# Kernel tuning notes

Measured on AMD Instinct MI355X. Metric: run time of the kernel, lower is better.

## Reference

```python
import jax, jax.numpy as jnp
import numpy as np

B, SQ, SKV = 4, 2048, 2048
IN_Q, IN_KV = 1024, 1024
H, D = 16, 64            # num_heads, hidden_channels (per-head dim)
OUT = 1024
ROPE_BASE = 4096.0


def _rope(x, base):
    # x: (..., items, D). Interleaved rotate-half RoPE over last dim.
    d = x.shape[-1]
    s = x.shape[-2]
    inv_freq = base ** (-jnp.arange(0, d, 2, dtype=x.dtype) / d)      # (D/2,)
    ang = jnp.arange(s, dtype=x.dtype)[:, None] * inv_freq[None, :]   # (S, D/2)
    cos = jnp.repeat(jnp.cos(ang), 2, axis=-1)                        # (S, D)
    sin = jnp.repeat(jnp.sin(ang), 2, axis=-1)
    xp = x.reshape(x.shape[:-1] + (d // 2, 2))
    x_rot = jnp.stack([-xp[..., 1], xp[..., 0]], axis=-1).reshape(x.shape)
    return x * cos + x_rot * sin


def setup_inputs() -> dict:
    key = jax.random.key(0)
    ks = jax.random.split(key, 8)
    sc = 0.02
    return {
        "q": jax.random.normal(ks[0], (B, SQ, IN_Q), jnp.float32),
        "kv": jax.random.normal(ks[1], (B, SKV, IN_KV), jnp.float32),
        # weights stored (in, out): y = x @ W + b  (equiv. to torch Linear)
        "Wq": jax.random.normal(ks[2], (IN_Q, H * D), jnp.float32) * sc,
        "bq": jnp.zeros((H * D,), jnp.float32),
        "Wkv": jax.random.normal(ks[3], (IN_KV, 2 * D), jnp.float32) * sc,
        "bkv": jnp.zeros((2 * D,), jnp.float32),
        "Wo": jax.random.normal(ks[4], (H * D, OUT), jnp.float32) * sc,
        "bo": jnp.zeros((OUT,), jnp.float32),
    }


def reference(q, kv, Wq, bq, Wkv, bkv, Wo, bo):
    # Q projection -> (B, H, SQ, D)
    qh = (q @ Wq + bq).reshape(B, SQ, H, D).transpose(0, 2, 1, 3)
    # KV projection (multi-query: single shared K/V head) -> (B, SKV, D) each
    kvp = kv @ Wkv + bkv
    k, v = kvp[..., :D], kvp[..., D:]
    # Rotary positional encoding on the item axis
    qh = _rope(qh, ROPE_BASE)
    k = _rope(k, ROPE_BASE)
    # Scaled dot-product attention with broadcast single-head K/V (MQA)
    scale = 1.0 / jnp.sqrt(jnp.asarray(D, qh.dtype))
    scores = jnp.einsum("bhqd,bkd->bhqk", qh, k) * scale   # (B,H,SQ,SKV)
    attn = jax.nn.softmax(scores, axis=-1)
    h = jnp.einsum("bhqk,bkd->bhqd", attn, v)              # (B,H,SQ,D)
    # Merge heads and output projection
    h = h.transpose(0, 2, 1, 3).reshape(B, SQ, H * D)
    return h @ Wo + bo
```

## Files before the change

### kernel.cpp

```cpp
#include <hip/hip_runtime.h>
#include <math.h>

typedef __bf16 bf16;
typedef __bf16 bf16x4 __attribute__((ext_vector_type(4)));
typedef __bf16 bf16x8 __attribute__((ext_vector_type(8)));
typedef float floatx4 __attribute__((ext_vector_type(4)));

#define MFMA16(a, b, c) __builtin_amdgcn_mfma_f32_16x16x32_bf16(a, b, c, 0, 0, 0)

#if __has_builtin(__builtin_amdgcn_exp2f)
#define EXP2F(x) __builtin_amdgcn_exp2f(x)
#else
#define EXP2F(x) exp2f(x)
#endif

constexpr int Bc = 4, SQc = 2048, SKVc = 2048, Hc = 16, Dc = 64;
#define QSCALE 0.18033688011112042f

__device__ __forceinline__ void glds16(const bf16* g, bf16* lds_base, int lane) {
#if __has_builtin(__builtin_amdgcn_global_load_lds)
  __builtin_amdgcn_global_load_lds(
      (const __attribute__((address_space(1))) void*)g,
      (__attribute__((address_space(3))) void*)lds_base, 16, 0, 0);
#else
  *(bf16x8*)(lds_base + 8 * lane) = *(const bf16x8*)g;
#endif
}

__global__ void cvt_bf16(const float* __restrict__ in, bf16* __restrict__ out) {
  const size_t i = ((size_t)blockIdx.x * 256 + threadIdx.x) * 4;
  const float4 v = *(const float4*)&in[i];
  bf16x4 o = {(bf16)v.x, (bf16)v.y, (bf16)v.z, (bf16)v.w};
  *(bf16x4*)&out[i] = o;
}

__global__ void rope_tab_build(float2* __restrict__ tab) {
  const int i = blockIdx.x * 256 + threadIdx.x;
  const int pos = i >> 5, f = i & 31;
  const float ang = (float)pos * exp2f(-0.375f * (float)f);
  float sn, cs;
  sincosf(ang, &sn, &cs);
  tab[i] = make_float2(cs, sn);
}

__global__ void transpose_cvt(const float* __restrict__ in, bf16* __restrict__ out,
                              int K, int N) {
  __shared__ bf16 T[64][72];
  const int tid = threadIdx.x;
  const int n0 = blockIdx.x * 64, k0 = blockIdx.y * 64;
  const int tr = tid >> 4, tc4 = (tid & 15) * 4;
#pragma unroll
  for (int i = 0; i < 4; i++) {
    const int k = tr + 16 * i;
    const float4 v = *(const float4*)&in[(size_t)(k0 + k) * N + n0 + tc4];
    T[tc4 + 0][k] = (bf16)v.x;
    T[tc4 + 1][k] = (bf16)v.y;
    T[tc4 + 2][k] = (bf16)v.z;
    T[tc4 + 3][k] = (bf16)v.w;
  }
  __syncthreads();
  const int nr = tid >> 2, kc = (tid & 3) * 8;
#pragma unroll
  for (int hf = 0; hf < 2; hf++)
    *(bf16x8*)&out[(size_t)(n0 + nr) * K + k0 + kc + 32 * hf] =
        *(const bf16x8*)&T[nr][kc + 32 * hf];
}

__device__ __forceinline__ void gemm_kloop(const bf16* __restrict__ A,
                                           const bf16* __restrict__ BT, int m0,
                                           int n0, int tid, int wave, int lane,
                                           int m, int g, bf16 (*As)[128 * 64],
                                           bf16 (*Bs)[128 * 64],
                                           floatx4 (*acc)[4], int mq, int nq) {
  const int r_ = tid >> 3, p_ = tid & 7;
  const bf16* pA[4];
  const bf16* pB[4];
#pragma unroll
  for (int q = 0; q < 4; q++) {
    const int r = r_ + q * 32;
    const int s = p_ ^ (r & 7);
    pA[q] = &A[(size_t)(m0 + r) * 1024 + 8 * s];
    pB[q] = &BT[(size_t)(n0 + r) * 1024 + 8 * s];
  }

#pragma unroll
  for (int q = 0; q < 4; q++) {
    glds16(pA[q], &As[0][(q * 4 + wave) * 512], lane);
    glds16(pB[q], &Bs[0][(q * 4 + wave) * 512], lane);
  }
  __syncthreads();

  for (int t = 0; t < 16; ++t) {
    const int cur = t & 1;
    if (t < 15) {
      const int k0 = 64 * (t + 1);
#pragma unroll
      for (int q = 0; q < 4; q++) {
        glds16(pA[q] + k0, &As[cur ^ 1][(q * 4 + wave) * 512], lane);
        glds16(pB[q] + k0, &Bs[cur ^ 1][(q * 4 + wave) * 512], lane);
      }
    }
    bf16x8 bb[4][2];
#pragma unroll
    for (int j = 0; j < 4; j++) {
      const int row = nq + 16 * j + m;
#pragma unroll
      for (int kh = 0; kh < 2; kh++)
        bb[j][kh] =
            *(const bf16x8*)&Bs[cur][row * 64 + 8 * ((g + 4 * kh) ^ (row & 7))];
    }
#pragma unroll
    for (int i = 0; i < 4; i++) {
      const int row = mq + 16 * i + m;
      const bf16x8 a0 = *(const bf16x8*)&As[cur][row * 64 + 8 * (g ^ (row & 7))];
      const bf16x8 a1 =
          *(const bf16x8*)&As[cur][row * 64 + 8 * ((g + 4) ^ (row & 7))];
#pragma unroll
      for (int j = 0; j < 4; j++) {
        acc[i][j] = MFMA16(a0, bb[j][0], acc[i][j]);
        acc[i][j] = MFMA16(a1, bb[j][1], acc[i][j]);
      }
    }
    __syncthreads();
  }
}

__global__ __launch_bounds__(256, 2) void gemm_qkv(
    const bf16* __restrict__ qA, const bf16* __restrict__ qBT,
    const float* __restrict__ qb, const bf16* __restrict__ kvA,
    const bf16* __restrict__ kvBT, const float* __restrict__ kvb,
    const float2* __restrict__ tab, bf16* __restrict__ qh,
    bf16* __restrict__ kko, bf16* __restrict__ vto) {
  __shared__ bf16 As[2][128 * 64];
  __shared__ bf16 Bs[2][128 * 64];

  const int tid = threadIdx.x, lane = tid & 63, wave = tid >> 6;
  const int m = lane & 15, g = lane >> 4;
  const int m0 = blockIdx.x * 128;
  const bool isQ = (blockIdx.y < 8);
  const int n0 = isQ ? blockIdx.y * 128 : 0;
  const bf16* A = isQ ? qA : kvA;
  const bf16* BT = isQ ? qBT : kvBT;
  const float* bias = isQ ? qb : kvb;
  const int mq = (wave >> 1) * 64, nq = (wave & 1) * 64;

  floatx4 z = {0.f, 0.f, 0.f, 0.f};
  floatx4 acc[4][4];
#pragma unroll
  for (int i = 0; i < 4; i++)
#pragma unroll
    for (int j = 0; j < 4; j++) acc[i][j] = z;

  gemm_kloop(A, BT, m0, n0, tid, wave, lane, m, g, As, Bs, acc, mq, nq);

  const int rq = 4 * g;
#pragma unroll
  for (int j = 0; j < 4; j++) {
    const int col = n0 + nq + 16 * j + m;
    const float bv = bias[col];
#pragma unroll
    for (int i = 0; i < 4; i++) {
#pragma unroll
      for (int r = 0; r < 4; r++) {
        const int row = m0 + mq + 16 * i + rq + r;
        float v = acc[i][j][r] + bv;
        const float vp = __shfl_xor(v, 1);
        if (isQ) {
          const int d = col & 63, hh = col >> 6;
          const int pos = row & (SQc - 1), b = row >> 11;
          const float2 cssn = tab[pos * 32 + (d >> 1)];
          const float res = (d & 1) ? (v * cssn.x + vp * cssn.y)
                                    : (v * cssn.x - vp * cssn.y);
          qh[(((size_t)(b * Hc + hh) * SQc) + pos) * Dc + d] = (bf16)(res * QSCALE);
        } else {
          const int pos = row & (SKVc - 1), b = row >> 11;
          const size_t fb = (size_t)b * (SKVc * Dc);
          if (col < 64) {
            const int d = col;
            const float2 cssn = tab[pos * 32 + (d >> 1)];
            const float res = (d & 1) ? (v * cssn.x + vp * cssn.y)
                                      : (v * cssn.x - vp * cssn.y);
            const int kc = (pos >> 4) * 2 + (d >> 5);
            const int kl = ((d >> 3) & 3) * 16 + (pos & 15);
            kko[fb + (size_t)kc * 512 + kl * 8 + (d & 7)] = (bf16)res;
          } else {
            const int d = col - 64;
            const int vc = (pos >> 6) * 8 + (d >> 4) * 2 + ((pos >> 5) & 1);
            const int vl = ((pos >> 3) & 3) * 16 + (d & 15);
            vto[fb + (size_t)vc * 512 + vl * 8 + (pos & 7)] = (bf16)v;
          }
        }
      }
    }
  }
}

__global__ __launch_bounds__(256, 2) void gemm_out(
    const bf16* __restrict__ A, const bf16* __restrict__ BT,
    const float* __restrict__ bias, float* __restrict__ out) {
  __shared__ bf16 As[2][128 * 64];
  __shared__ bf16 Bs[2][128 * 64];

  const int tid = threadIdx.x, lane = tid & 63, wave = tid >> 6;
  const int m = lane & 15, g = lane >> 4;
  const int m0 = blockIdx.x * 128, n0 = blockIdx.y * 128;
  const int mq = (wave >> 1) * 64, nq = (wave & 1) * 64;

  floatx4 z = {0.f, 0.f, 0.f, 0.f};
  floatx4 acc[4][4];
#pragma unroll
  for (int i = 0; i < 4; i++)
#pragma unroll
    for (int j = 0; j < 4; j++) acc[i][j] = z;

  gemm_kloop(A, BT, m0, n0, tid, wave, lane, m, g, As, Bs, acc, mq, nq);

  const int rq = 4 * g;
#pragma unroll
  for (int j = 0; j < 4; j++) {
    const int col = n0 + nq + 16 * j + m;
    const float bv = bias[col];
#pragma unroll
    for (int i = 0; i < 4; i++)
#pragma unroll
      for (int r = 0; r < 4; r++) {
        const int row = m0 + mq + 16 * i + rq + r;
        out[(size_t)row * 1024 + col] = acc[i][j][r] + bv;
      }
  }
}

__global__ __launch_bounds__(512, 4) void attn_v5(
    const bf16* __restrict__ qh, const bf16* __restrict__ kk,
    const bf16* __restrict__ vt, bf16* __restrict__ hout) {
  const int bid = blockIdx.x;
  const int qt = bid & 7, h = (bid >> 3) & 15, b = bid >> 7;
  const int tid = threadIdx.x, lane = tid & 63, wave = tid >> 6;
  const int m = lane & 15, g = lane >> 4;

  __shared__ bf16 Kb[2][4096];
  __shared__ bf16 Vb[4096];
  __shared__ bf16 Pb[8][2][16][68];

  const int q0 = qt * 256 + wave * 32;
  const bf16* qp = qh + (((size_t)(b * Hc + h) * SQc) + q0 + m) * Dc + 8 * g;
  bf16x8 bq[2][2];
#pragma unroll
  for (int s = 0; s < 2; s++) {
    bq[s][0] = *(const bf16x8*)(qp + (size_t)(16 * s) * Dc);
    bq[s][1] = *(const bf16x8*)(qp + (size_t)(16 * s) * Dc + 32);
  }

  const bf16 one = (bf16)1.0f;
  const bf16x8 ones = {one, one, one, one, one, one, one, one};

  floatx4 z = {0.f, 0.f, 0.f, 0.f};
  floatx4 accO[2][4];
  floatx4 lacc[2] = {z, z};
#pragma unroll
  for (int s = 0; s < 2; s++)
#pragma unroll
    for (int t = 0; t < 4; t++) accO[s][t] = z;

  const size_t fb = (size_t)b * (SKVc * Dc);
  const bf16* kg = kk + fb + 8 * lane;
  const bf16* vg = vt + fb + 8 * lane;

  glds16(kg + (size_t)wave * 512, &Kb[0][wave * 512], lane);
  __syncthreads();

  for (int it = 0; it < 32; ++it) {
    const int cur = it & 1;
    if (it) __syncthreads();
    glds16(vg + (size_t)(it * 8 + wave) * 512, &Vb[wave * 512], lane);
    if (it + 1 < 32)
      glds16(kg + (size_t)((it + 1) * 8 + wave) * 512, &Kb[cur ^ 1][wave * 512],
             lane);

    bf16x8 kfr[4][2];
#pragma unroll
    for (int c = 0; c < 4; c++) {
      kfr[c][0] = *(const bf16x8*)&Kb[cur][(2 * c + 0) * 512 + 8 * lane];
      kfr[c][1] = *(const bf16x8*)&Kb[cur][(2 * c + 1) * 512 + 8 * lane];
    }
#pragma unroll
    for (int s = 0; s < 2; s++) {
#pragma unroll
      for (int c = 0; c < 4; c++) {
        floatx4 sv = MFMA16(kfr[c][0], bq[s][0], z);
        sv = MFMA16(kfr[c][1], bq[s][1], sv);
        bf16x4 pk = {(bf16)EXP2F(sv[0]), (bf16)EXP2F(sv[1]), (bf16)EXP2F(sv[2]),
                     (bf16)EXP2F(sv[3])};
        *(bf16x4*)&Pb[wave][s][m][16 * c + 4 * g] = pk;
      }
    }
    __syncthreads();

    bf16x8 vf[4][2];
#pragma unroll
    for (int t = 0; t < 4; t++) {
      vf[t][0] = *(const bf16x8*)&Vb[(2 * t + 0) * 512 + 8 * lane];
      vf[t][1] = *(const bf16x8*)&Vb[(2 * t + 1) * 512 + 8 * lane];
    }
#pragma unroll
    for (int s = 0; s < 2; s++) {
      const bf16x8 pa0 = *(const bf16x8*)&Pb[wave][s][m][8 * g];
      const bf16x8 pa1 = *(const bf16x8*)&Pb[wave][s][m][32 + 8 * g];
      lacc[s] = MFMA16(pa0, ones, lacc[s]);
      lacc[s] = MFMA16(pa1, ones, lacc[s]);
#pragma unroll
      for (int t = 0; t < 4; t++) {
        accO[s][t] = MFMA16(pa0, vf[t][0], accO[s][t]);
        accO[s][t] = MFMA16(pa1, vf[t][1], accO[s][t]);
      }
    }
  }

#pragma unroll
  for (int s = 0; s < 2; s++) {
    floatx4 inv;
#pragma unroll
    for (int r = 0; r < 4; r++) inv[r] = 1.0f / lacc[s][r];
#pragma unroll
    for (int t = 0; t < 4; t++)
#pragma unroll
      for (int r = 0; r < 4; r++) {
        const int qrow = q0 + 16 * s + 4 * g + r;
        hout[((size_t)(b * SQc + qrow)) * (Hc * Dc) + h * Dc + 16 * t + m] =
            (bf16)(accO[s][t][r] * inv[r]);
      }
  }
}

extern "C" void kernel_launch(void* const* d_in, const int* in_sizes, int n_in,
                              void* d_out, int out_size, void* d_ws, size_t ws_size,
                              hipStream_t stream) {
  const float* q = (const float*)d_in[0];
  const float* kv = (const float*)d_in[1];
  const float* Wq = (const float*)d_in[2];
  const float* bq = (const float*)d_in[3];
  const float* Wkv = (const float*)d_in[4];
  const float* bkv = (const float*)d_in[5];
  const float* Wo = (const float*)d_in[6];
  const float* bo = (const float*)d_in[7];

  char* ws = (char*)d_ws;
  bf16* qbf = (bf16*)ws;
  bf16* kvbf = (bf16*)(ws + ((size_t)16 << 20));
  bf16* WqT = (bf16*)(ws + ((size_t)32 << 20));
  bf16* WkvT = (bf16*)(ws + ((size_t)34 << 20));
  float2* rtab = (float2*)(ws + ((size_t)34 << 20) + ((size_t)256 << 10));
  bf16* WoT = (bf16*)(ws + ((size_t)35 << 20));
  bf16* qh = (bf16*)(ws + ((size_t)37 << 20));
  bf16* kk = (bf16*)(ws + ((size_t)53 << 20));
  bf16* vt = (bf16*)(ws + ((size_t)54 << 20));
  bf16* hh = qbf;

  const int M = Bc * SQc;

  rope_tab_build<<<256, 256, 0, stream>>>(rtab);
  cvt_bf16<<<M, 256, 0, stream>>>(q, qbf);
  cvt_bf16<<<M, 256, 0, stream>>>(kv, kvbf);
  transpose_cvt<<<dim3(16, 16), 256, 0, stream>>>(Wq, WqT, 1024, 1024);
  transpose_cvt<<<dim3(2, 16), 256, 0, stream>>>(Wkv, WkvT, 1024, 128);
  transpose_cvt<<<dim3(16, 16), 256, 0, stream>>>(Wo, WoT, 1024, 1024);

  gemm_qkv<<<dim3(64, 9), 256, 0, stream>>>(qbf, WqT, bq, kvbf, WkvT, bkv, rtab,
                                            qh, kk, vt);
  attn_v5<<<Bc * Hc * (SQc / 256), 512, 0, stream>>>(qh, kk, vt, hh);
  gemm_out<<<dim3(64, 8), 256, 0, stream>>>(hh, WoT, bo, (float*)d_out);
}
```

Before: 284.9 us.

## Replace double-buffered GEMM LDS pipeline with single buffer and raise occupancy

The projection GEMM k-loop drops its double-buffered shared-memory prefetch and uses a single buffer with a barrier before and after each tile load. This halves LDS per block (64KB to 32KB), and launch bounds go from 2 to 3 blocks per CU for both GEMM kernels. The aim is to hide global-load latency through more resident blocks rather than in-block prefetch. The cost is that loads no longer overlap MFMA work within a block, and the tighter register budget may cause spills.

```diff
diff --git a/kernel.cpp b/kernel.cpp
--- a/kernel.cpp
+++ b/kernel.cpp
@@ -69,8 +69,7 @@
 __device__ __forceinline__ void gemm_kloop(const bf16* __restrict__ A,
                                            const bf16* __restrict__ BT, int m0,
                                            int n0, int tid, int wave, int lane,
-                                           int m, int g, bf16 (*As)[128 * 64],
-                                           bf16 (*Bs)[128 * 64],
+                                           int m, int g, bf16* As, bf16* Bs,
                                            floatx4 (*acc)[4], int mq, int nq) {
   const int r_ = tid >> 3, p_ = tid & 7;
   const bf16* pA[4];
@@ -83,56 +82,45 @@
     pB[q] = &BT[(size_t)(n0 + r) * 1024 + 8 * s];
   }
 
-#pragma unroll
-  for (int q = 0; q < 4; q++) {
-    glds16(pA[q], &As[0][(q * 4 + wave) * 512], lane);
-    glds16(pB[q], &Bs[0][(q * 4 + wave) * 512], lane);
-  }
-  __syncthreads();
-
-  for (int t = 0; t < 16; ++t) {
-    const int cur = t & 1;
-    if (t < 15) {
-      const int k0 = 64 * (t + 1);
-#pragma unroll
-      for (int q = 0; q < 4; q++) {
-        glds16(pA[q] + k0, &As[cur ^ 1][(q * 4 + wave) * 512], lane);
-        glds16(pB[q] + k0, &Bs[cur ^ 1][(q * 4 + wave) * 512], lane);
-      }
-    }
+  for (int k0 = 0; k0 < 1024; k0 += 64) {
+    __syncthreads();
+#pragma unroll
+    for (int q = 0; q < 4; q++) {
+      glds16(pA[q] + k0, &As[(q * 4 + wave) * 512], lane);
+      glds16(pB[q] + k0, &Bs[(q * 4 + wave) * 512], lane);
+    }
+    __syncthreads();
+
     bf16x8 bb[4][2];
 #pragma unroll
     for (int j = 0; j < 4; j++) {
       const int row = nq + 16 * j + m;
 #pragma unroll
       for (int kh = 0; kh < 2; kh++)
-        bb[j][kh] =
-            *(const bf16x8*)&Bs[cur][row * 64 + 8 * ((g + 4 * kh) ^ (row & 7))];
+        bb[j][kh] = *(const bf16x8*)&Bs[row * 64 + 8 * ((g + 4 * kh) ^ (row & 7))];
     }
 #pragma unroll
     for (int i = 0; i < 4; i++) {
       const int row = mq + 16 * i + m;
-      const bf16x8 a0 = *(const bf16x8*)&As[cur][row * 64 + 8 * (g ^ (row & 7))];
-      const bf16x8 a1 =
-          *(const bf16x8*)&As[cur][row * 64 + 8 * ((g + 4) ^ (row & 7))];
+      const bf16x8 a0 = *(const bf16x8*)&As[row * 64 + 8 * (g ^ (row & 7))];
+      const bf16x8 a1 = *(const bf16x8*)&As[row * 64 + 8 * ((g + 4) ^ (row & 7))];
 #pragma unroll
       for (int j = 0; j < 4; j++) {
         acc[i][j] = MFMA16(a0, bb[j][0], acc[i][j]);
         acc[i][j] = MFMA16(a1, bb[j][1], acc[i][j]);
       }
     }
-    __syncthreads();
-  }
-}
-
-__global__ __launch_bounds__(256, 2) void gemm_qkv(
+  }
+}
+
+__global__ __launch_bounds__(256, 3) void gemm_qkv(
     const bf16* __restrict__ qA, const bf16* __restrict__ qBT,
     const float* __restrict__ qb, const bf16* __restrict__ kvA,
     const bf16* __restrict__ kvBT, const float* __restrict__ kvb,
     const float2* __restrict__ tab, bf16* __restrict__ qh,
     bf16* __restrict__ kko, bf16* __restrict__ vto) {
-  __shared__ bf16 As[2][128 * 64];
-  __shared__ bf16 Bs[2][128 * 64];
+  __shared__ bf16 As[128 * 64];
+  __shared__ bf16 Bs[128 * 64];
 
   const int tid = threadIdx.x, lane = tid & 63, wave = tid >> 6;
   const int m = lane & 15, g = lane >> 4;
@@ -195,11 +183,11 @@
   }
 }
 
-__global__ __launch_bounds__(256, 2) void gemm_out(
+__global__ __launch_bounds__(256, 3) void gemm_out(
     const bf16* __restrict__ A, const bf16* __restrict__ BT,
     const float* __restrict__ bias, float* __restrict__ out) {
-  __shared__ bf16 As[2][128 * 64];
-  __shared__ bf16 Bs[2][128 * 64];
+  __shared__ bf16 As[128 * 64];
+  __shared__ bf16 Bs[128 * 64];
 
   const int tid = threadIdx.x, lane = tid & 63, wave = tid >> 6;
   const int m = lane & 15, g = lane >> 4;
```

Measured after the change: 261.4 us. -8.2%, faster.
